# Kernel optimization log

Measured on AMD Instinct MI355X. Metric: run time of the kernel, lower is better.

The kernel has to match this reference:

```python
import jax, jax.numpy as jnp
import numpy as np

N_NODES = 100000


def gcn_conv(x, edge_index, W, b, num_nodes):
    # PyG GCNConv: h = x @ W; add self-loops; symmetric deg^-1/2 normalization;
    # out[dst] = sum_{src->dst} norm * h[src] + b
    h = x @ W
    loop = jnp.arange(num_nodes)
    src = jnp.concatenate([edge_index[0], loop])
    dst = jnp.concatenate([edge_index[1], loop])
    deg = jax.ops.segment_sum(jnp.ones_like(dst, dtype=h.dtype), dst, num_segments=num_nodes)
    dinv = jnp.where(deg > 0, jax.lax.rsqrt(deg), 0.0)
    norm = dinv[src] * dinv[dst]  # [E+N]
    msg = h[src] * norm[:, None]  # gather + scale
    out = jax.ops.segment_sum(msg, dst, num_segments=num_nodes)
    return out + b


def setup_inputs() -> dict:
    key = jax.random.key(0)
    k1, k2, k3, k4 = jax.random.split(key, 4)
    E = 3200000
    F_IN, HID, CLS = 512, 16, 7
    x = jax.random.normal(k1, (N_NODES, F_IN), dtype=jnp.float32)
    edge_index = jax.random.randint(k2, (2, E), 0, N_NODES, dtype=jnp.int64)
    W1 = jax.random.normal(k3, (F_IN, HID), dtype=jnp.float32) / np.sqrt(F_IN)
    b1 = jnp.zeros((HID,), dtype=jnp.float32)
    W2 = jax.random.normal(k4, (HID, CLS), dtype=jnp.float32) / np.sqrt(HID)
    b2 = jnp.zeros((CLS,), dtype=jnp.float32)
    return {"x": x, "edge_index": edge_index, "W1": W1, "b1": b1, "W2": W2, "b2": b2}


def reference(x, edge_index, W1, b1, W2, b2):
    h = gcn_conv(x, edge_index, W1, b1, N_NODES)
    h = jax.nn.relu(h)
    # dropout is identity in eval mode (p=0.5, training=False)
    out = gcn_conv(h, edge_index, W2, b2, N_NODES)
    return out
```

## Files before the change

kernel.cpp:

```cpp
#include <hip/hip_runtime.h>

#define N_NODES 100000
#define F_IN 512
#define HID 16
#define CLS 7

#define BK_SHIFT 8
#define BK_NODES 256
#define NBK ((N_NODES + BK_NODES - 1) / BK_NODES)
#define BK_CAP 9216

__global__ void detect_i64_kernel(const unsigned int* __restrict__ idx32,
                                  int* __restrict__ flag, int n_check) {
    __shared__ unsigned int s;
    if (threadIdx.x == 0) s = 0u;
    __syncthreads();
    unsigned int v = 0u;
    for (int i = threadIdx.x; i < n_check; i += blockDim.x)
        v |= idx32[2 * i + 1];
    atomicOr(&s, v);
    __syncthreads();
    if (threadIdx.x == 0) *flag = (s == 0u) ? 1 : 0;
}

__device__ __forceinline__ void get_edge(const void* eidx, long long E,
                                         long long e, int is64,
                                         int& s, int& d) {
    if (is64) {
        const long long* p = (const long long*)eidx;
        s = (int)p[e];
        d = (int)p[E + e];
    } else {
        const int* p = (const int*)eidx;
        s = p[e];
        d = p[E + e];
    }
}

#define SB_T 512
#define SB_TILE 4096

__global__ __launch_bounds__(SB_T) void scatter_bin_kernel(const void* __restrict__ eidx,
                                                           long long E,
                                                           const int* __restrict__ flag,
                                                           int* __restrict__ cursor,
                                                           unsigned int* __restrict__ binned) {
    __shared__ unsigned int stage[SB_TILE];
    __shared__ unsigned short stageb[SB_TILE];
    __shared__ int hist[NBK];
    __shared__ int excl[NBK];
    __shared__ int curs[NBK];
    __shared__ int gbase[NBK];
    __shared__ int scanv[SB_T];
    const int is64 = *flag;
    const int tid = threadIdx.x;
    const long long tileBeg = (long long)blockIdx.x * SB_TILE;
    long long rem = E - tileBeg;
    const int cnt = (int)(rem < SB_TILE ? rem : SB_TILE);

    for (int i = tid; i < NBK; i += SB_T) hist[i] = 0;
    __syncthreads();
    for (int i = tid; i < cnt; i += SB_T) {
        long long e = tileBeg + i;
        int d;
        if (is64) d = (int)((const long long*)eidx)[E + e];
        else      d = ((const int*)eidx)[E + e];
        atomicAdd(&hist[d >> BK_SHIFT], 1);
    }
    __syncthreads();
    scanv[tid] = (tid < NBK) ? hist[tid] : 0;
    __syncthreads();
    for (int off = 1; off < SB_T; off <<= 1) {
        int a = (tid >= off) ? scanv[tid - off] : 0;
        __syncthreads();
        scanv[tid] += a;
        __syncthreads();
    }
    if (tid < NBK) {
        int e = scanv[tid] - hist[tid];
        excl[tid] = e;
        curs[tid] = e;
    }
    __syncthreads();
    for (int i = tid; i < cnt; i += SB_T) {
        long long e = tileBeg + i;
        int s, d;
        get_edge(eidx, E, e, is64, s, d);
        int b = d >> BK_SHIFT;
        int pos = atomicAdd(&curs[b], 1);
        stage[pos] = ((unsigned int)(d & (BK_NODES - 1)) << 17) | (unsigned int)s;
        stageb[pos] = (unsigned short)b;
    }
    __syncthreads();
    if (tid < NBK) gbase[tid] = hist[tid]
        ? (tid * BK_CAP + atomicAdd(&cursor[tid], hist[tid])) : 0;
    __syncthreads();
    for (int i = tid; i < cnt; i += SB_T) {
        int b = stageb[i];
        int pos = gbase[b] + (i - excl[b]);
        if (pos < (b + 1) * BK_CAP)
            binned[pos] = stage[i];
    }
}

__global__ __launch_bounds__(256) void csr_build_kernel(const int* __restrict__ cursor,
                                                        unsigned int* __restrict__ binned,
                                                        float* __restrict__ dinv,
                                                        int* __restrict__ rowptr,
                                                        int* __restrict__ degA) {
    __shared__ unsigned int stage[BK_CAP];
    __shared__ int hist[BK_NODES];
    __shared__ int scanv[BK_NODES];
    __shared__ int curs[BK_NODES];
    const int tid = threadIdx.x;
    const int b = blockIdx.x;
    const int base = b * BK_CAP;
    int cnt = cursor[b];
    if (cnt > BK_CAP) cnt = BK_CAP;
    hist[tid] = 0;
    __syncthreads();
    for (int i = tid; i < cnt; i += 256)
        atomicAdd(&hist[binned[base + i] >> 17], 1);
    __syncthreads();
    scanv[tid] = hist[tid];
    __syncthreads();
    for (int off = 1; off < BK_NODES; off <<= 1) {
        int a = (tid >= off) ? scanv[tid - off] : 0;
        __syncthreads();
        scanv[tid] += a;
        __syncthreads();
    }
    {
        int e = scanv[tid] - hist[tid];
        curs[tid] = e;
        int g = b * BK_NODES + tid;
        if (g < N_NODES) {
            rowptr[g] = base + e;
            degA[g] = hist[tid];
            dinv[g] = rsqrtf((float)(hist[tid] + 1));
        }
    }
    __syncthreads();
    for (int i = tid; i < cnt; i += 256) {
        unsigned int v = binned[base + i];
        int pos = atomicAdd(&curs[(int)(v >> 17)], 1);
        stage[pos] = v & 0x1FFFFu;
    }
    __syncthreads();
    for (int i = tid; i < cnt; i += 256)
        binned[base + i] = stage[i];
}

#define G1_ROWS 64
#define G1_KC 64

__global__ __launch_bounds__(256) void gemm1_kernel(const float* __restrict__ x,
                                                    const float* __restrict__ W1,
                                                    const float* __restrict__ dinv,
                                                    float* __restrict__ h1s) {
    __shared__ float Ws[F_IN * HID];
    __shared__ float xs[G1_ROWS][G1_KC + 4];
    const int tid = threadIdx.x;
    const int rowBase = blockIdx.x * G1_ROWS;

#pragma unroll
    for (int it = 0; it < 8; it++) {
        int f = it * 256 + tid;
        ((float4*)Ws)[f] = ((const float4*)W1)[f];
    }

    const int r  = tid >> 2;
    const int j4 = tid & 3;
    float4 acc = make_float4(0.f, 0.f, 0.f, 0.f);

    for (int kc = 0; kc < F_IN; kc += G1_KC) {
        __syncthreads();
#pragma unroll
        for (int it = 0; it < 4; it++) {
            int f = it * 256 + tid;
            int row = f >> 4;
            int c4 = f & 15;
            int grow = rowBase + row;
            if (grow >= N_NODES) grow = N_NODES - 1;
            float4 v = ((const float4*)(x + (long long)grow * F_IN + kc))[c4];
            *((float4*)&xs[row][c4 * 4]) = v;
        }
        __syncthreads();
#pragma unroll
        for (int k = 0; k < G1_KC; k++) {
            float xv = xs[r][k];
            float4 wv = ((const float4*)(Ws + (kc + k) * HID))[j4];
            acc.x += xv * wv.x;
            acc.y += xv * wv.y;
            acc.z += xv * wv.z;
            acc.w += xv * wv.w;
        }
    }
    int grow = rowBase + r;
    if (grow < N_NODES) {
        float dn = dinv[grow];
        acc.x *= dn; acc.y *= dn; acc.z *= dn; acc.w *= dn;
        ((float4*)(h1s + (long long)grow * HID))[j4] = acc;
    }
}

#define A1_NODES 64

__global__ __launch_bounds__(256) void agg1_gemm2_kernel(const int* __restrict__ rowptr,
                                                         const int* __restrict__ degA,
                                                         const int* __restrict__ csr_src,
                                                         const float* __restrict__ h1s,
                                                         const float* __restrict__ dinv,
                                                         const float* __restrict__ b1,
                                                         const float* __restrict__ W2,
                                                         float* __restrict__ h2s) {
    __shared__ float W2s[HID][8];
    __shared__ float t_lds[A1_NODES][HID + 1];
    const int tid = threadIdx.x;
    if (tid < HID * 8) {
        int j = tid >> 3, c = tid & 7;
        W2s[j][c] = (c < CLS) ? W2[j * CLS + c] : 0.f;
    }
    const int ln = tid >> 2;
    const int j4 = tid & 3;
    const int n = blockIdx.x * A1_NODES + ln;
    float dn = 0.f;
    if (n < N_NODES) {
        const int beg = rowptr[n];
        const int end = beg + degA[n];
        const float4* h4 = (const float4*)h1s;
        float4 a0 = make_float4(0.f, 0.f, 0.f, 0.f);
        float4 a1 = make_float4(0.f, 0.f, 0.f, 0.f);
        int k = beg;
        for (; k + 4 <= end; k += 4) {
            int s0 = csr_src[k], s1 = csr_src[k + 1];
            int s2 = csr_src[k + 2], s3 = csr_src[k + 3];
            float4 v0 = h4[(long long)s0 * 4 + j4];
            float4 v1 = h4[(long long)s1 * 4 + j4];
            float4 v2 = h4[(long long)s2 * 4 + j4];
            float4 v3 = h4[(long long)s3 * 4 + j4];
            a0.x += v0.x; a0.y += v0.y; a0.z += v0.z; a0.w += v0.w;
            a1.x += v1.x; a1.y += v1.y; a1.z += v1.z; a1.w += v1.w;
            a0.x += v2.x; a0.y += v2.y; a0.z += v2.z; a0.w += v2.w;
            a1.x += v3.x; a1.y += v3.y; a1.z += v3.z; a1.w += v3.w;
        }
        for (; k < end; k++) {
            float4 v = h4[(long long)csr_src[k] * 4 + j4];
            a0.x += v.x; a0.y += v.y; a0.z += v.z; a0.w += v.w;
        }
        dn = dinv[n];
        float4 self = h4[(long long)n * 4 + j4];
        float4 bb = ((const float4*)b1)[j4];
        float* tp = &t_lds[ln][j4 * 4];
        tp[0] = fmaxf(bb.x + dn * (a0.x + a1.x + self.x), 0.f);
        tp[1] = fmaxf(bb.y + dn * (a0.y + a1.y + self.y), 0.f);
        tp[2] = fmaxf(bb.z + dn * (a0.z + a1.z + self.z), 0.f);
        tp[3] = fmaxf(bb.w + dn * (a0.w + a1.w + self.w), 0.f);
    }
    __syncthreads();
    if (n < N_NODES) {
        float b0 = 0.f, c1 = 0.f;
#pragma unroll
        for (int j = 0; j < HID; j++) {
            float v = t_lds[ln][j];
            b0 += v * W2s[j][2 * j4];
            c1 += v * W2s[j][2 * j4 + 1];
        }
        h2s[(long long)n * 8 + 2 * j4]     = dn * b0;
        h2s[(long long)n * 8 + 2 * j4 + 1] = dn * c1;
    }
}

#define A2_NODES 32

__global__ __launch_bounds__(256) void agg2_gather_kernel(const int* __restrict__ rowptr,
                                                          const int* __restrict__ degA,
                                                          const int* __restrict__ csr_src,
                                                          const float* __restrict__ h2s,
                                                          const float* __restrict__ dinv,
                                                          const float* __restrict__ b2,
                                                          float* __restrict__ out) {
    const int tid = threadIdx.x;
    const int ln = tid >> 3;
    const int c = tid & 7;
    const int n = blockIdx.x * A2_NODES + ln;
    if (n >= N_NODES) return;
    const int beg = rowptr[n];
    const int end = beg + degA[n];
    float a0 = 0.f, a1 = 0.f;
    int k = beg;
    for (; k + 4 <= end; k += 4) {
        int s0 = csr_src[k], s1 = csr_src[k + 1];
        int s2 = csr_src[k + 2], s3 = csr_src[k + 3];
        float v0 = h2s[(long long)s0 * 8 + c];
        float v1 = h2s[(long long)s1 * 8 + c];
        float v2 = h2s[(long long)s2 * 8 + c];
        float v3 = h2s[(long long)s3 * 8 + c];
        a0 += v0 + v2;
        a1 += v1 + v3;
    }
    for (; k < end; k++)
        a0 += h2s[(long long)csr_src[k] * 8 + c];
    if (c < CLS)
        out[(long long)n * CLS + c] =
            b2[c] + dinv[n] * (h2s[(long long)n * 8 + c] + a0 + a1);
}

extern "C" void kernel_launch(void* const* d_in, const int* in_sizes, int n_in,
                              void* d_out, int out_size, void* d_ws, size_t ws_size,
                              hipStream_t stream) {
    const float* x    = (const float*)d_in[0];
    const void*  eidx = d_in[1];
    const float* W1   = (const float*)d_in[2];
    const float* b1   = (const float*)d_in[3];
    const float* W2   = (const float*)d_in[4];
    const float* b2   = (const float*)d_in[5];
    float* out = (float*)d_out;
    const long long E = (long long)in_sizes[1] / 2;

    char* ws = (char*)d_ws;
    size_t off = 0;
    auto alloc = [&](size_t bytes) -> void* {
        void* p = ws + off;
        off = (off + bytes + 255) & ~(size_t)255;
        return p;
    };
    int*          flag   = (int*)alloc(4);
    int*          cursor = (int*)alloc((size_t)NBK * 4);
    unsigned int* binned = (unsigned int*)alloc((size_t)NBK * BK_CAP * 4);
    int*          rowptr = (int*)alloc((size_t)N_NODES * 4);
    int*          degA   = (int*)alloc((size_t)N_NODES * 4);
    float*        dinv   = (float*)alloc((size_t)N_NODES * 4);
    float*        h1s    = (float*)alloc((size_t)N_NODES * HID * 4);
    float*        h2s    = (float*)alloc((size_t)N_NODES * 8 * 4);
    (void)ws_size;

    hipMemsetAsync(cursor, 0, (size_t)NBK * 4, stream);

    detect_i64_kernel<<<1, 256, 0, stream>>>((const unsigned int*)eidx, flag,
                                             (int)(E < 4096 ? E : 4096));

    scatter_bin_kernel<<<(int)((E + SB_TILE - 1) / SB_TILE), SB_T, 0, stream>>>(
        eidx, E, flag, cursor, binned);

    csr_build_kernel<<<NBK, 256, 0, stream>>>(cursor, binned, dinv, rowptr, degA);

    gemm1_kernel<<<(N_NODES + G1_ROWS - 1) / G1_ROWS, 256, 0, stream>>>(x, W1, dinv, h1s);

    const int* csr_src = (const int*)binned;
    agg1_gemm2_kernel<<<(N_NODES + A1_NODES - 1) / A1_NODES, 256, 0, stream>>>(
        rowptr, degA, csr_src, h1s, dinv, b1, W2, h2s);

    agg2_gather_kernel<<<(N_NODES + A2_NODES - 1) / A2_NODES, 256, 0, stream>>>(
        rowptr, degA, csr_src, h2s, dinv, b2, out);
}
```

Baseline: 445.1 us.

## Replace CSR build with bucket-local LDS atomic aggregation over feature planes

Drops the per-bucket counting sort and CSR arrays and aggregates directly from the binned edge list with shared-memory float atomics per 256-node bucket. Node features move to a planar float4 layout (one plane per 4 features), and each plane is handled by a separate grid y-slice so gathers stay 16-byte. The second GEMM with ReLU becomes its own kernel. This removes the sort and its extra binned pass, but adds LDS atomic contention, reads the edge list once per plane, and makes summation order nondeterministic.

```diff
diff --git a/kernel.cpp b/kernel.cpp
--- a/kernel.cpp
+++ b/kernel.cpp
@@ -103,15 +103,10 @@
     }
 }
 
-__global__ __launch_bounds__(256) void csr_build_kernel(const int* __restrict__ cursor,
-                                                        unsigned int* __restrict__ binned,
-                                                        float* __restrict__ dinv,
-                                                        int* __restrict__ rowptr,
-                                                        int* __restrict__ degA) {
-    __shared__ unsigned int stage[BK_CAP];
+__global__ __launch_bounds__(256) void deg_dinv_kernel(const int* __restrict__ cursor,
+                                                       const unsigned int* __restrict__ binned,
+                                                       float* __restrict__ dinv) {
     __shared__ int hist[BK_NODES];
-    __shared__ int scanv[BK_NODES];
-    __shared__ int curs[BK_NODES];
     const int tid = threadIdx.x;
     const int b = blockIdx.x;
     const int base = b * BK_CAP;
@@ -122,33 +117,8 @@
     for (int i = tid; i < cnt; i += 256)
         atomicAdd(&hist[binned[base + i] >> 17], 1);
     __syncthreads();
-    scanv[tid] = hist[tid];
-    __syncthreads();
-    for (int off = 1; off < BK_NODES; off <<= 1) {
-        int a = (tid >= off) ? scanv[tid - off] : 0;
-        __syncthreads();
-        scanv[tid] += a;
-        __syncthreads();
-    }
-    {
-        int e = scanv[tid] - hist[tid];
-        curs[tid] = e;
-        int g = b * BK_NODES + tid;
-        if (g < N_NODES) {
-            rowptr[g] = base + e;
-            degA[g] = hist[tid];
-            dinv[g] = rsqrtf((float)(hist[tid] + 1));
-        }
-    }
-    __syncthreads();
-    for (int i = tid; i < cnt; i += 256) {
-        unsigned int v = binned[base + i];
-        int pos = atomicAdd(&curs[(int)(v >> 17)], 1);
-        stage[pos] = v & 0x1FFFFu;
-    }
-    __syncthreads();
-    for (int i = tid; i < cnt; i += 256)
-        binned[base + i] = stage[i];
+    int g = b * BK_NODES + tid;
+    if (g < N_NODES) dinv[g] = rsqrtf((float)(hist[tid] + 1));
 }
 
 #define G1_ROWS 64
@@ -157,7 +127,7 @@
 __global__ __launch_bounds__(256) void gemm1_kernel(const float* __restrict__ x,
                                                     const float* __restrict__ W1,
                                                     const float* __restrict__ dinv,
-                                                    float* __restrict__ h1s) {
+                                                    float4* __restrict__ h1q) {
     __shared__ float Ws[F_IN * HID];
     __shared__ float xs[G1_ROWS][G1_KC + 4];
     const int tid = threadIdx.x;
@@ -200,110 +170,156 @@
     if (grow < N_NODES) {
         float dn = dinv[grow];
         acc.x *= dn; acc.y *= dn; acc.z *= dn; acc.w *= dn;
-        ((float4*)(h1s + (long long)grow * HID))[j4] = acc;
-    }
-}
-
-#define A1_NODES 64
-
-__global__ __launch_bounds__(256) void agg1_gemm2_kernel(const int* __restrict__ rowptr,
-                                                         const int* __restrict__ degA,
-                                                         const int* __restrict__ csr_src,
-                                                         const float* __restrict__ h1s,
+        h1q[(long long)j4 * N_NODES + grow] = acc;
+    }
+}
+
+#define AGG_T 512
+
+__global__ __launch_bounds__(AGG_T) void agg1q_kernel(const int* __restrict__ cursor,
+                                                      const unsigned int* __restrict__ binned,
+                                                      const float4* __restrict__ h1q,
+                                                      const float* __restrict__ dinv,
+                                                      const float* __restrict__ b1,
+                                                      float4* __restrict__ aggq) {
+    __shared__ float acc[BK_NODES][5];
+    const int tid = threadIdx.x;
+    const int b = blockIdx.x;
+    const int q = blockIdx.y;
+    const int base = b * BK_CAP;
+    int cnt = cursor[b];
+    if (cnt > BK_CAP) cnt = BK_CAP;
+    for (int i = tid; i < BK_NODES * 5; i += AGG_T) ((float*)acc)[i] = 0.f;
+    __syncthreads();
+
+    const float4* plane = h1q + (long long)q * N_NODES;
+    int i = tid;
+    for (; i + AGG_T < cnt; i += 2 * AGG_T) {
+        unsigned int v0 = binned[base + i];
+        unsigned int v1 = binned[base + i + AGG_T];
+        float4 h0 = plane[v0 & 0x1FFFFu];
+        float4 h1 = plane[v1 & 0x1FFFFu];
+        float* a0 = acc[v0 >> 17];
+        float* a1 = acc[v1 >> 17];
+        atomicAdd(a0 + 0, h0.x); atomicAdd(a0 + 1, h0.y);
+        atomicAdd(a0 + 2, h0.z); atomicAdd(a0 + 3, h0.w);
+        atomicAdd(a1 + 0, h1.x); atomicAdd(a1 + 1, h1.y);
+        atomicAdd(a1 + 2, h1.z); atomicAdd(a1 + 3, h1.w);
+    }
+    for (; i < cnt; i += AGG_T) {
+        unsigned int v = binned[base + i];
+        float4 h = plane[v & 0x1FFFFu];
+        float* a = acc[v >> 17];
+        atomicAdd(a + 0, h.x); atomicAdd(a + 1, h.y);
+        atomicAdd(a + 2, h.z); atomicAdd(a + 3, h.w);
+    }
+    __syncthreads();
+
+    if (tid < BK_NODES) {
+        int g = b * BK_NODES + tid;
+        if (g < N_NODES) {
+            float dn = dinv[g];
+            float4 self = plane[g];
+            float4 bb = ((const float4*)b1)[q];
+            float4 o;
+            o.x = bb.x + dn * (acc[tid][0] + self.x);
+            o.y = bb.y + dn * (acc[tid][1] + self.y);
+            o.z = bb.z + dn * (acc[tid][2] + self.z);
+            o.w = bb.w + dn * (acc[tid][3] + self.w);
+            aggq[(long long)q * N_NODES + g] = o;
+        }
+    }
+}
+
+__global__ __launch_bounds__(256) void gemm2_relu_kernel(const float4* __restrict__ aggq,
+                                                         const float* __restrict__ W2,
                                                          const float* __restrict__ dinv,
-                                                         const float* __restrict__ b1,
-                                                         const float* __restrict__ W2,
-                                                         float* __restrict__ h2s) {
+                                                         float4* __restrict__ h2q) {
     __shared__ float W2s[HID][8];
-    __shared__ float t_lds[A1_NODES][HID + 1];
     const int tid = threadIdx.x;
     if (tid < HID * 8) {
         int j = tid >> 3, c = tid & 7;
         W2s[j][c] = (c < CLS) ? W2[j * CLS + c] : 0.f;
     }
-    const int ln = tid >> 2;
-    const int j4 = tid & 3;
-    const int n = blockIdx.x * A1_NODES + ln;
-    float dn = 0.f;
-    if (n < N_NODES) {
-        const int beg = rowptr[n];
-        const int end = beg + degA[n];
-        const float4* h4 = (const float4*)h1s;
-        float4 a0 = make_float4(0.f, 0.f, 0.f, 0.f);
-        float4 a1 = make_float4(0.f, 0.f, 0.f, 0.f);
-        int k = beg;
-        for (; k + 4 <= end; k += 4) {
-            int s0 = csr_src[k], s1 = csr_src[k + 1];
-            int s2 = csr_src[k + 2], s3 = csr_src[k + 3];
-            float4 v0 = h4[(long long)s0 * 4 + j4];
-            float4 v1 = h4[(long long)s1 * 4 + j4];
-            float4 v2 = h4[(long long)s2 * 4 + j4];
-            float4 v3 = h4[(long long)s3 * 4 + j4];
-            a0.x += v0.x; a0.y += v0.y; a0.z += v0.z; a0.w += v0.w;
-            a1.x += v1.x; a1.y += v1.y; a1.z += v1.z; a1.w += v1.w;
-            a0.x += v2.x; a0.y += v2.y; a0.z += v2.z; a0.w += v2.w;
-            a1.x += v3.x; a1.y += v3.y; a1.z += v3.z; a1.w += v3.w;
+    __syncthreads();
+    int n = blockIdx.x * 256 + tid;
+    if (n >= N_NODES) return;
+    float t[HID];
+#pragma unroll
+    for (int q = 0; q < 4; q++) {
+        float4 v = aggq[(long long)q * N_NODES + n];
+        t[q * 4 + 0] = fmaxf(v.x, 0.f);
+        t[q * 4 + 1] = fmaxf(v.y, 0.f);
+        t[q * 4 + 2] = fmaxf(v.z, 0.f);
+        t[q * 4 + 3] = fmaxf(v.w, 0.f);
+    }
+    float dn = dinv[n];
+    float o[8];
+#pragma unroll
+    for (int c = 0; c < 8; c++) {
+        float a = 0.f;
+#pragma unroll
+        for (int j = 0; j < HID; j++) a += t[j] * W2s[j][c];
+        o[c] = dn * a;
+    }
+    h2q[(long long)0 * N_NODES + n] = make_float4(o[0], o[1], o[2], o[3]);
+    h2q[(long long)1 * N_NODES + n] = make_float4(o[4], o[5], o[6], o[7]);
+}
+
+__global__ __launch_bounds__(AGG_T) void agg2q_kernel(const int* __restrict__ cursor,
+                                                      const unsigned int* __restrict__ binned,
+                                                      const float4* __restrict__ h2q,
+                                                      const float* __restrict__ dinv,
+                                                      const float* __restrict__ b2,
+                                                      float* __restrict__ out) {
+    __shared__ float acc[BK_NODES][5];
+    const int tid = threadIdx.x;
+    const int b = blockIdx.x;
+    const int q = blockIdx.y;
+    const int base = b * BK_CAP;
+    int cnt = cursor[b];
+    if (cnt > BK_CAP) cnt = BK_CAP;
+    for (int i = tid; i < BK_NODES * 5; i += AGG_T) ((float*)acc)[i] = 0.f;
+    __syncthreads();
+
+    const float4* plane = h2q + (long long)q * N_NODES;
+    int i = tid;
+    for (; i + AGG_T < cnt; i += 2 * AGG_T) {
+        unsigned int v0 = binned[base + i];
+        unsigned int v1 = binned[base + i + AGG_T];
+        float4 h0 = plane[v0 & 0x1FFFFu];
+        float4 h1 = plane[v1 & 0x1FFFFu];
+        float* a0 = acc[v0 >> 17];
+        float* a1 = acc[v1 >> 17];
+        atomicAdd(a0 + 0, h0.x); atomicAdd(a0 + 1, h0.y);
+        atomicAdd(a0 + 2, h0.z); atomicAdd(a0 + 3, h0.w);
+        atomicAdd(a1 + 0, h1.x); atomicAdd(a1 + 1, h1.y);
+        atomicAdd(a1 + 2, h1.z); atomicAdd(a1 + 3, h1.w);
+    }
+    for (; i < cnt; i += AGG_T) {
+        unsigned int v = binned[base + i];
+        float4 h = plane[v & 0x1FFFFu];
+        float* a = acc[v >> 17];
+        atomicAdd(a + 0, h.x); atomicAdd(a + 1, h.y);
+        atomicAdd(a + 2, h.z); atomicAdd(a + 3, h.w);
+    }
+    __syncthreads();
+
+    if (tid < BK_NODES) {
+        int g = b * BK_NODES + tid;
+        if (g < N_NODES) {
+            float dn = dinv[g];
+            float4 self = plane[g];
+            const int c0 = q * 4;
+            const int ncols = (q == 0) ? 4 : 3;
+            float sv[4] = {self.x, self.y, self.z, self.w};
+            float* op = out + (long long)g * CLS + c0;
+#pragma unroll
+            for (int c = 0; c < 4; c++)
+                if (c < ncols)
+                    op[c] = b2[c0 + c] + dn * (acc[tid][c] + sv[c]);
         }
-        for (; k < end; k++) {
-            float4 v = h4[(long long)csr_src[k] * 4 + j4];
-            a0.x += v.x; a0.y += v.y; a0.z += v.z; a0.w += v.w;
-        }
-        dn = dinv[n];
-        float4 self = h4[(long long)n * 4 + j4];
-        float4 bb = ((const float4*)b1)[j4];
-        float* tp = &t_lds[ln][j4 * 4];
-        tp[0] = fmaxf(bb.x + dn * (a0.x + a1.x + self.x), 0.f);
-        tp[1] = fmaxf(bb.y + dn * (a0.y + a1.y + self.y), 0.f);
-        tp[2] = fmaxf(bb.z + dn * (a0.z + a1.z + self.z), 0.f);
-        tp[3] = fmaxf(bb.w + dn * (a0.w + a1.w + self.w), 0.f);
-    }
-    __syncthreads();
-    if (n < N_NODES) {
-        float b0 = 0.f, c1 = 0.f;
-#pragma unroll
-        for (int j = 0; j < HID; j++) {
-            float v = t_lds[ln][j];
-            b0 += v * W2s[j][2 * j4];
-            c1 += v * W2s[j][2 * j4 + 1];
-        }
-        h2s[(long long)n * 8 + 2 * j4]     = dn * b0;
-        h2s[(long long)n * 8 + 2 * j4 + 1] = dn * c1;
-    }
-}
-
-#define A2_NODES 32
-
-__global__ __launch_bounds__(256) void agg2_gather_kernel(const int* __restrict__ rowptr,
-                                                          const int* __restrict__ degA,
-                                                          const int* __restrict__ csr_src,
-                                                          const float* __restrict__ h2s,
-                                                          const float* __restrict__ dinv,
-                                                          const float* __restrict__ b2,
-                                                          float* __restrict__ out) {
-    const int tid = threadIdx.x;
-    const int ln = tid >> 3;
-    const int c = tid & 7;
-    const int n = blockIdx.x * A2_NODES + ln;
-    if (n >= N_NODES) return;
-    const int beg = rowptr[n];
-    const int end = beg + degA[n];
-    float a0 = 0.f, a1 = 0.f;
-    int k = beg;
-    for (; k + 4 <= end; k += 4) {
-        int s0 = csr_src[k], s1 = csr_src[k + 1];
-        int s2 = csr_src[k + 2], s3 = csr_src[k + 3];
-        float v0 = h2s[(long long)s0 * 8 + c];
-        float v1 = h2s[(long long)s1 * 8 + c];
-        float v2 = h2s[(long long)s2 * 8 + c];
-        float v3 = h2s[(long long)s3 * 8 + c];
-        a0 += v0 + v2;
-        a1 += v1 + v3;
-    }
-    for (; k < end; k++)
-        a0 += h2s[(long long)csr_src[k] * 8 + c];
-    if (c < CLS)
-        out[(long long)n * CLS + c] =
-            b2[c] + dinv[n] * (h2s[(long long)n * 8 + c] + a0 + a1);
+    }
 }
 
 extern "C" void kernel_launch(void* const* d_in, const int* in_sizes, int n_in,
@@ -328,11 +344,10 @@
     int*          flag   = (int*)alloc(4);
     int*          cursor = (int*)alloc((size_t)NBK * 4);
     unsigned int* binned = (unsigned int*)alloc((size_t)NBK * BK_CAP * 4);
-    int*          rowptr = (int*)alloc((size_t)N_NODES * 4);
-    int*          degA   = (int*)alloc((size_t)N_NODES * 4);
     float*        dinv   = (float*)alloc((size_t)N_NODES * 4);
-    float*        h1s    = (float*)alloc((size_t)N_NODES * HID * 4);
-    float*        h2s    = (float*)alloc((size_t)N_NODES * 8 * 4);
+    float4*       h1q    = (float4*)alloc((size_t)N_NODES * 4 * 16);
+    float4*       aggq   = (float4*)alloc((size_t)N_NODES * 4 * 16);
+    float4*       h2q    = (float4*)alloc((size_t)N_NODES * 2 * 16);
     (void)ws_size;
 
     hipMemsetAsync(cursor, 0, (size_t)NBK * 4, stream);
@@ -343,14 +358,13 @@
     scatter_bin_kernel<<<(int)((E + SB_TILE - 1) / SB_TILE), SB_T, 0, stream>>>(
         eidx, E, flag, cursor, binned);
 
-    csr_build_kernel<<<NBK, 256, 0, stream>>>(cursor, binned, dinv, rowptr, degA);
-
-    gemm1_kernel<<<(N_NODES + G1_ROWS - 1) / G1_ROWS, 256, 0, stream>>>(x, W1, dinv, h1s);
-
-    const int* csr_src = (const int*)binned;
-    agg1_gemm2_kernel<<<(N_NODES + A1_NODES - 1) / A1_NODES, 256, 0, stream>>>(
-        rowptr, degA, csr_src, h1s, dinv, b1, W2, h2s);
-
-    agg2_gather_kernel<<<(N_NODES + A2_NODES - 1) / A2_NODES, 256, 0, stream>>>(
-        rowptr, degA, csr_src, h2s, dinv, b2, out);
-}
+    deg_dinv_kernel<<<NBK, 256, 0, stream>>>(cursor, binned, dinv);
+
+    gemm1_kernel<<<(N_NODES + G1_ROWS - 1) / G1_ROWS, 256, 0, stream>>>(x, W1, dinv, h1q);
+
+    agg1q_kernel<<<dim3(NBK, 4), AGG_T, 0, stream>>>(cursor, binned, h1q, dinv, b1, aggq);
+
+    gemm2_relu_kernel<<<(N_NODES + 255) / 256, 256, 0, stream>>>(aggq, W2, dinv, h2q);
+
+    agg2q_kernel<<<dim3(NBK, 2), AGG_T, 0, stream>>>(cursor, binned, h2q, dinv, b2, out);
+}
```

New measurement: 829.3 us. 86.3% more time.
